# Kernel tuning notes

Measured on AMD Instinct MI355X. Metric: run time of the kernel, lower is better.

Reference implementation:

```python
import jax, jax.numpy as jnp
import numpy as np

# norse.LIFCell default parameters
DT = 1e-3
TAU_SYN_INV = 200.0   # 1 / 5e-3
TAU_MEM_INV = 100.0   # 1 / 1e-2
V_TH = 1.0
V_LEAK = 0.0
V_RESET = 0.0
ALPHA = 100.0         # SuperSpike surrogate slope

T, B, N_IN, N_HIDDEN, N_OUT = 16, 4096, 784, 256, 10


@jax.custom_vjp
def heaviside(x):
    return (x > 0).astype(x.dtype)

def _h_fwd(x):
    return heaviside(x), x

def _h_bwd(x, g):
    # SuperSpike surrogate: d/dx H(x) ~ 1 / (alpha*|x| + 1)^2
    return (g / (ALPHA * jnp.abs(x) + 1.0) ** 2,)

heaviside.defvjp(_h_fwd, _h_bwd)


def lif_step(inp, v, i):
    """One norse lif_step: Euler-integrate v and i, spike, hard reset."""
    v_decayed = v + DT * TAU_MEM_INV * ((V_LEAK - v) + i)
    i_decayed = i - DT * TAU_SYN_INV * i
    z = heaviside(v_decayed - V_TH)
    v_new = (1.0 - z) * v_decayed + z * V_RESET
    i_new = i_decayed + inp
    return z, v_new, i_new


def setup_inputs() -> dict:
    key = jax.random.key(0)
    k1, k2, k3, k4, k5 = jax.random.split(key, 5)
    # binary spike trains (T, B, N_IN)
    spike_input = (jax.random.uniform(k1, (T, B, N_IN)) < 0.3).astype(jnp.float32)
    lim1 = float(1.0 / np.sqrt(N_IN))
    lim2 = float(1.0 / np.sqrt(N_HIDDEN))
    W1 = jax.random.uniform(k2, (N_HIDDEN, N_IN), minval=-lim1, maxval=lim1, dtype=jnp.float32)
    b1 = jax.random.uniform(k3, (N_HIDDEN,), minval=-lim1, maxval=lim1, dtype=jnp.float32)
    W2 = jax.random.uniform(k4, (N_OUT, N_HIDDEN), minval=-lim2, maxval=lim2, dtype=jnp.float32)
    b2 = jax.random.uniform(k5, (N_OUT,), minval=-lim2, maxval=lim2, dtype=jnp.float32)
    return {"spike_input": spike_input, "W1": W1, "b1": b1, "W2": W2, "b2": b2}


def reference(spike_input, W1, b1, W2, b2):
    batch = spike_input.shape[1]
    nh, no = W1.shape[0], W2.shape[0]
    dtype = spike_input.dtype
    # LIFCell with state=None starts at v=v_leak, i=0
    init = (jnp.full((batch, nh), V_LEAK, dtype), jnp.zeros((batch, nh), dtype),
            jnp.full((batch, no), V_LEAK, dtype), jnp.zeros((batch, no), dtype))

    def step(carry, x_t):
        v1, i1, v2, i2 = carry
        c1 = x_t @ W1.T + b1                 # (B, N_HIDDEN)
        z1, v1, i1 = lif_step(c1, v1, i1)
        c2 = z1 @ W2.T + b2                  # (B, N_OUT)
        z2, v2, i2 = lif_step(c2, v2, i2)
        return (v1, i1, v2, i2), z2

    _, zs = jax.lax.scan(step, init, spike_input)  # zs: (T, B, N_OUT)
    return zs.sum(axis=0)                          # (B, N_OUT)
```

## Files before the change

### kernel.cpp

```cpp
#include <hip/hip_runtime.h>


#define T_STEPS 16
#define B_SZ    4096
#define N_IN    784
#define N_HID   256
#define N_OUT   10
#define M_TOT   (T_STEPS * B_SZ)
#define KPAD    800

typedef __bf16 bf16x8 __attribute__((ext_vector_type(8)));
typedef float  f32x4  __attribute__((ext_vector_type(4)));
typedef unsigned short ushort_t;

__device__ __forceinline__ unsigned short bf16_rne(float f) {
    unsigned u = __builtin_bit_cast(unsigned, f);
    u += 0x7fffu + ((u >> 16) & 1u);
    return (unsigned short)(u >> 16);
}

__global__ __launch_bounds__(256) void conv_w(
    const float* __restrict__ W1,
    unsigned short* __restrict__ Whi, unsigned short* __restrict__ Wlo)
{
    const int idx = blockIdx.x * 256 + threadIdx.x;
    if (idx >= N_HID * KPAD) return;
    const int n = idx / KPAD, k = idx % KPAD;
    unsigned short h = 0, l = 0;
    if (k < N_IN) {
        const float w = W1[n * N_IN + k];
        h = bf16_rne(w);
        const float hf = __builtin_bit_cast(float, (unsigned)h << 16);
        l = bf16_rne(w - hf);
    }
    Whi[idx] = h;
    Wlo[idx] = l;
}

__global__ __launch_bounds__(512, 4) void gemm1_mfma(
    const float* __restrict__ X,
    const unsigned short* __restrict__ Whi,
    const unsigned short* __restrict__ Wlo,
    const float* __restrict__ b1,
    float* __restrict__ C)
{
    __shared__ ushort_t As[2][128 * 32];
    __shared__ ushort_t Bh[2][256 * 32];
    __shared__ ushort_t Bl[2][256 * 32];

    const int tid  = threadIdx.x;
    const int lane = tid & 63;
    const int w    = tid >> 6;
    const int wm   = w >> 2;
    const int wn   = w & 3;
    const int m0   = blockIdx.x * 128;

    const int ar  = tid >> 2;
    const int ap  = tid & 3;
    const int acs = ap ^ (ar & 3);
    const float* aSrc = X + (size_t)(m0 + ar) * N_IN + acs * 8;

    f32x4 acc[4][4];
    #pragma unroll
    for (int i = 0; i < 4; ++i)
        #pragma unroll
        for (int j = 0; j < 4; ++j)
            #pragma unroll
            for (int q = 0; q < 4; ++q)
                acc[i][j][q] = 0.0f;

    auto stage = [&](int bi, int kt) {
        const int k0 = kt * 32;
        #pragma unroll
        for (int ii = 0; ii < 2; ++ii) {
            const int rb = w * 32 + ii * 16 + (lane >> 2);
            const int cs = (lane & 3) ^ (rb & 3);
            const size_t go = (size_t)rb * KPAD + k0 + cs * 8;
            ushort_t* dh = &Bh[bi][(w * 32 + ii * 16) * 32];
            ushort_t* dl = &Bl[bi][(w * 32 + ii * 16) * 32];
            __builtin_amdgcn_global_load_lds(
                (const __attribute__((address_space(1))) void*)(Whi + go),
                (__attribute__((address_space(3))) void*)dh, 16, 0, 0);
            __builtin_amdgcn_global_load_lds(
                (const __attribute__((address_space(1))) void*)(Wlo + go),
                (__attribute__((address_space(3))) void*)dl, 16, 0, 0);
        }
        const int kg = k0 + acs * 8;
        uint4 pk = make_uint4(0u, 0u, 0u, 0u);
        if (kg < N_IN) {
            const float4* s = reinterpret_cast<const float4*>(aSrc + k0);
            const float4 f0 = s[0];
            const float4 f1 = s[1];
            pk.x = (__builtin_bit_cast(unsigned, f0.x) >> 16) |
                   (__builtin_bit_cast(unsigned, f0.y) & 0xffff0000u);
            pk.y = (__builtin_bit_cast(unsigned, f0.z) >> 16) |
                   (__builtin_bit_cast(unsigned, f0.w) & 0xffff0000u);
            pk.z = (__builtin_bit_cast(unsigned, f1.x) >> 16) |
                   (__builtin_bit_cast(unsigned, f1.y) & 0xffff0000u);
            pk.w = (__builtin_bit_cast(unsigned, f1.z) >> 16) |
                   (__builtin_bit_cast(unsigned, f1.w) & 0xffff0000u);
        }
        *reinterpret_cast<uint4*>(&As[bi][ar * 32 + ap * 8]) = pk;
    };

    const int NT = KPAD / 32;
    int buf = 0;
    stage(0, 0);

    for (int kt = 0; kt < NT; ++kt) {
        __syncthreads();

        bf16x8 af[4];
        #pragma unroll
        for (int i = 0; i < 4; ++i) {
            const int r = wm * 64 + i * 16 + (lane & 15);
            const int p = (lane >> 4) ^ (r & 3);
            af[i] = *reinterpret_cast<const bf16x8*>(&As[buf][r * 32 + p * 8]);
        }
        bf16x8 bfr[4];
        #pragma unroll
        for (int j = 0; j < 4; ++j) {
            const int r = wn * 64 + j * 16 + (lane & 15);
            const int p = (lane >> 4) ^ (r & 3);
            bfr[j] = *reinterpret_cast<const bf16x8*>(&Bh[buf][r * 32 + p * 8]);
        }

        if (kt + 1 < NT) stage(buf ^ 1, kt + 1);

        #pragma unroll
        for (int i = 0; i < 4; ++i)
            #pragma unroll
            for (int j = 0; j < 4; ++j)
                acc[i][j] = __builtin_amdgcn_mfma_f32_16x16x32_bf16(
                    af[i], bfr[j], acc[i][j], 0, 0, 0);

        #pragma unroll
        for (int j = 0; j < 4; ++j) {
            const int r = wn * 64 + j * 16 + (lane & 15);
            const int p = (lane >> 4) ^ (r & 3);
            bfr[j] = *reinterpret_cast<const bf16x8*>(&Bl[buf][r * 32 + p * 8]);
        }
        #pragma unroll
        for (int i = 0; i < 4; ++i)
            #pragma unroll
            for (int j = 0; j < 4; ++j)
                acc[i][j] = __builtin_amdgcn_mfma_f32_16x16x32_bf16(
                    af[i], bfr[j], acc[i][j], 0, 0, 0);

        buf ^= 1;
    }

    #pragma unroll
    for (int j = 0; j < 4; ++j) {
        const int col  = wn * 64 + j * 16 + (lane & 15);
        const float bb = b1[col];
        #pragma unroll
        for (int i = 0; i < 4; ++i) {
            const int rbase = m0 + wm * 64 + i * 16 + ((lane >> 4) << 2);
            #pragma unroll
            for (int q = 0; q < 4; ++q)
                C[(size_t)(rbase + q) * N_HID + col] = acc[i][j][q] + bb;
        }
    }
}

__global__ __launch_bounds__(256) void lif1_kernel(float* __restrict__ C1)
{
    const int g = blockIdx.x * 256 + threadIdx.x;
    const size_t stride = (size_t)B_SZ * N_HID;
    float v = 0.0f, cur = 0.0f;
    #pragma unroll
    for (int t = 0; t < T_STEPS; ++t) {
        const size_t off = (size_t)t * stride + g;
        const float c = C1[off];
        const float vd = v + 0.1f * ((0.0f - v) + cur);
        const float id = cur - 0.2f * cur;
        const bool  sp = vd > 1.0f;
        C1[off] = sp ? 1.0f : 0.0f;
        v = sp ? 0.0f : vd;
        cur = id + c;
    }
}

__global__ __launch_bounds__(640) void gemm2_f32(
    const float* __restrict__ Z, const float* __restrict__ W2,
    const float* __restrict__ b2, float* __restrict__ C2)
{
    __shared__ float zs[64 * 268];
    __shared__ float ws[N_OUT * N_HID];
    const int tid = threadIdx.x;
    const int m0 = blockIdx.x * 64;

    for (int idx = tid; idx < 4096; idx += 640) {
        const int r = idx >> 6;
        const int c = (idx & 63) << 2;
        *(float4*)&zs[r * 268 + c] =
            *(const float4*)&Z[(size_t)(m0 + r) * N_HID + c];
    }
    *(float4*)&ws[tid * 4] = *(const float4*)&W2[tid * 4];
    __syncthreads();

    const int o = tid >> 6;
    const int r = tid & 63;
    float acc = b2[o];
    #pragma unroll
    for (int k = 0; k < N_HID; k += 4) {
        const float4 z4 = *(const float4*)&zs[r * 268 + k];
        const float4 w4 = *(const float4*)&ws[o * N_HID + k];
        acc += z4.x * w4.x + z4.y * w4.y + z4.z * w4.z + z4.w * w4.w;
    }
    C2[(size_t)(m0 + r) * N_OUT + o] = acc;
}

__global__ __launch_bounds__(256) void lif2_kernel(
    const float* __restrict__ C2, float* __restrict__ out)
{
    const int g = blockIdx.x * 256 + threadIdx.x;
    const int stride = B_SZ * N_OUT;
    float v = 0.0f, cur = 0.0f, s = 0.0f;
    #pragma unroll
    for (int t = 0; t < T_STEPS; ++t) {
        const float c = C2[t * stride + g];
        const float vd = v + 0.1f * ((0.0f - v) + cur);
        const float id = cur - 0.2f * cur;
        const bool  sp = vd > 1.0f;
        s += sp ? 1.0f : 0.0f;
        v = sp ? 0.0f : vd;
        cur = id + c;
    }
    out[g] = s;
}

extern "C" void kernel_launch(void* const* d_in, const int* in_sizes, int n_in,
                              void* d_out, int out_size, void* d_ws, size_t ws_size,
                              hipStream_t stream)
{
    const float* X  = (const float*)d_in[0];
    const float* W1 = (const float*)d_in[1];
    const float* b1 = (const float*)d_in[2];
    const float* W2 = (const float*)d_in[3];
    const float* b2 = (const float*)d_in[4];
    float* out = (float*)d_out;

    unsigned short* Whi = (unsigned short*)d_ws;
    unsigned short* Wlo = Whi + N_HID * KPAD;
    float* C1 = (float*)((char*)d_ws + (1 << 20));
    float* C2 = C1 + (size_t)M_TOT * N_HID;

    conv_w<<<(N_HID * KPAD + 255) / 256, 256, 0, stream>>>(W1, Whi, Wlo);

    gemm1_mfma<<<M_TOT / 128, 512, 0, stream>>>(X, Whi, Wlo, b1, C1);

    lif1_kernel<<<(B_SZ * N_HID) / 256, 256, 0, stream>>>(C1);

    gemm2_f32<<<M_TOT / 64, 640, 0, stream>>>(C1, W2, b2, C2);

    lif2_kernel<<<(B_SZ * N_OUT) / 256, 256, 0, stream>>>(C2, out);
}
```

Before: 132.1 us.

## Load GEMM1 operands directly from global into registers, dropping LDS staging

After: 216.6 us. 1.64x slower.

```diff
diff --git a/kernel.cpp b/kernel.cpp
--- a/kernel.cpp
+++ b/kernel.cpp
@@ -8,20 +8,22 @@
 #define N_OUT   10
 #define M_TOT   (T_STEPS * B_SZ)
 #define KPAD    800
+#define BKS     32
 
 typedef __bf16 bf16x8 __attribute__((ext_vector_type(8)));
 typedef float  f32x4  __attribute__((ext_vector_type(4)));
 typedef unsigned short ushort_t;
+typedef unsigned int   u32;
 
 __device__ __forceinline__ unsigned short bf16_rne(float f) {
-    unsigned u = __builtin_bit_cast(unsigned, f);
+    u32 u = __builtin_bit_cast(u32, f);
     u += 0x7fffu + ((u >> 16) & 1u);
     return (unsigned short)(u >> 16);
 }
 
 __global__ __launch_bounds__(256) void conv_w(
     const float* __restrict__ W1,
-    unsigned short* __restrict__ Whi, unsigned short* __restrict__ Wlo)
+    ushort_t* __restrict__ Whi, ushort_t* __restrict__ Wlo)
 {
     const int idx = blockIdx.x * 256 + threadIdx.x;
     if (idx >= N_HID * KPAD) return;
@@ -30,35 +32,46 @@
     if (k < N_IN) {
         const float w = W1[n * N_IN + k];
         h = bf16_rne(w);
-        const float hf = __builtin_bit_cast(float, (unsigned)h << 16);
+        const float hf = __builtin_bit_cast(float, (u32)h << 16);
         l = bf16_rne(w - hf);
     }
     Whi[idx] = h;
     Wlo[idx] = l;
 }
 
-__global__ __launch_bounds__(512, 4) void gemm1_mfma(
+__device__ __forceinline__ u32 pack_hi16(u32 a, u32 b) {
+    return (a >> 16) | (b & 0xffff0000u);
+}
+
+__global__ __launch_bounds__(512, 2) void gemm1_mfma(
     const float* __restrict__ X,
-    const unsigned short* __restrict__ Whi,
-    const unsigned short* __restrict__ Wlo,
+    const ushort_t* __restrict__ Whi,
+    const ushort_t* __restrict__ Wlo,
     const float* __restrict__ b1,
     float* __restrict__ C)
 {
-    __shared__ ushort_t As[2][128 * 32];
-    __shared__ ushort_t Bh[2][256 * 32];
-    __shared__ ushort_t Bl[2][256 * 32];
-
     const int tid  = threadIdx.x;
     const int lane = tid & 63;
     const int w    = tid >> 6;
     const int wm   = w >> 2;
     const int wn   = w & 3;
     const int m0   = blockIdx.x * 128;
-
-    const int ar  = tid >> 2;
-    const int ap  = tid & 3;
-    const int acs = ap ^ (ar & 3);
-    const float* aSrc = X + (size_t)(m0 + ar) * N_IN + acs * 8;
+    const int ls   = lane >> 4;
+    const int lr   = lane & 15;
+
+    const float* aP[4];
+    #pragma unroll
+    for (int i = 0; i < 4; ++i)
+        aP[i] = X + (size_t)(m0 + wm * 64 + i * 16 + lr) * N_IN + ls * 8;
+
+    const ushort_t* bhP[4];
+    const ushort_t* blP[4];
+    #pragma unroll
+    for (int j = 0; j < 4; ++j) {
+        const size_t ro = (size_t)(wn * 64 + j * 16 + lr) * KPAD + ls * 8;
+        bhP[j] = Whi + ro;
+        blP[j] = Wlo + ro;
+    }
 
     f32x4 acc[4][4];
     #pragma unroll
@@ -69,94 +82,55 @@
             for (int q = 0; q < 4; ++q)
                 acc[i][j][q] = 0.0f;
 
-    auto stage = [&](int bi, int kt) {
-        const int k0 = kt * 32;
-        #pragma unroll
-        for (int ii = 0; ii < 2; ++ii) {
-            const int rb = w * 32 + ii * 16 + (lane >> 2);
-            const int cs = (lane & 3) ^ (rb & 3);
-            const size_t go = (size_t)rb * KPAD + k0 + cs * 8;
-            ushort_t* dh = &Bh[bi][(w * 32 + ii * 16) * 32];
-            ushort_t* dl = &Bl[bi][(w * 32 + ii * 16) * 32];
-            __builtin_amdgcn_global_load_lds(
-                (const __attribute__((address_space(1))) void*)(Whi + go),
-                (__attribute__((address_space(3))) void*)dh, 16, 0, 0);
-            __builtin_amdgcn_global_load_lds(
-                (const __attribute__((address_space(1))) void*)(Wlo + go),
-                (__attribute__((address_space(3))) void*)dl, 16, 0, 0);
+    auto kstep = [&](int kt, bool tail) {
+        const int k0 = kt * BKS;
+        bf16x8 af[4];
+        #pragma unroll
+        for (int i = 0; i < 4; ++i) {
+            uint4 pk = make_uint4(0u, 0u, 0u, 0u);
+            if (!tail || ls < 2) {
+                const uint4* s = reinterpret_cast<const uint4*>(aP[i] + k0);
+                const uint4 q0 = s[0];
+                const uint4 q1 = s[1];
+                pk.x = pack_hi16(q0.x, q0.y);
+                pk.y = pack_hi16(q0.z, q0.w);
+                pk.z = pack_hi16(q1.x, q1.y);
+                pk.w = pack_hi16(q1.z, q1.w);
+            }
+            af[i] = __builtin_bit_cast(bf16x8, pk);
         }
-        const int kg = k0 + acs * 8;
-        uint4 pk = make_uint4(0u, 0u, 0u, 0u);
-        if (kg < N_IN) {
-            const float4* s = reinterpret_cast<const float4*>(aSrc + k0);
-            const float4 f0 = s[0];
-            const float4 f1 = s[1];
-            pk.x = (__builtin_bit_cast(unsigned, f0.x) >> 16) |
-                   (__builtin_bit_cast(unsigned, f0.y) & 0xffff0000u);
-            pk.y = (__builtin_bit_cast(unsigned, f0.z) >> 16) |
-                   (__builtin_bit_cast(unsigned, f0.w) & 0xffff0000u);
-            pk.z = (__builtin_bit_cast(unsigned, f1.x) >> 16) |
-                   (__builtin_bit_cast(unsigned, f1.y) & 0xffff0000u);
-            pk.w = (__builtin_bit_cast(unsigned, f1.z) >> 16) |
-                   (__builtin_bit_cast(unsigned, f1.w) & 0xffff0000u);
+        bf16x8 bh[4], bl[4];
+        #pragma unroll
+        for (int j = 0; j < 4; ++j) {
+            bh[j] = *reinterpret_cast<const bf16x8*>(bhP[j] + k0);
+            bl[j] = *reinterpret_cast<const bf16x8*>(blP[j] + k0);
         }
-        *reinterpret_cast<uint4*>(&As[bi][ar * 32 + ap * 8]) = pk;
-    };
-
-    const int NT = KPAD / 32;
-    int buf = 0;
-    stage(0, 0);
-
-    for (int kt = 0; kt < NT; ++kt) {
-        __syncthreads();
-
-        bf16x8 af[4];
-        #pragma unroll
-        for (int i = 0; i < 4; ++i) {
-            const int r = wm * 64 + i * 16 + (lane & 15);
-            const int p = (lane >> 4) ^ (r & 3);
-            af[i] = *reinterpret_cast<const bf16x8*>(&As[buf][r * 32 + p * 8]);
-        }
-        bf16x8 bfr[4];
-        #pragma unroll
-        for (int j = 0; j < 4; ++j) {
-            const int r = wn * 64 + j * 16 + (lane & 15);
-            const int p = (lane >> 4) ^ (r & 3);
-            bfr[j] = *reinterpret_cast<const bf16x8*>(&Bh[buf][r * 32 + p * 8]);
-        }
-
-        if (kt + 1 < NT) stage(buf ^ 1, kt + 1);
-
         #pragma unroll
         for (int i = 0; i < 4; ++i)
             #pragma unroll
             for (int j = 0; j < 4; ++j)
                 acc[i][j] = __builtin_amdgcn_mfma_f32_16x16x32_bf16(
-                    af[i], bfr[j], acc[i][j], 0, 0, 0);
-
-        #pragma unroll
-        for (int j = 0; j < 4; ++j) {
-            const int r = wn * 64 + j * 16 + (lane & 15);
-            const int p = (lane >> 4) ^ (r & 3);
-            bfr[j] = *reinterpret_cast<const bf16x8*>(&Bl[buf][r * 32 + p * 8]);
-        }
+                    af[i], bh[j], acc[i][j], 0, 0, 0);
         #pragma unroll
         for (int i = 0; i < 4; ++i)
             #pragma unroll
             for (int j = 0; j < 4; ++j)
                 acc[i][j] = __builtin_amdgcn_mfma_f32_16x16x32_bf16(
-                    af[i], bfr[j], acc[i][j], 0, 0, 0);
-
-        buf ^= 1;
-    }
+                    af[i], bl[j], acc[i][j], 0, 0, 0);
+    };
+
+    #pragma unroll 4
+    for (int kt = 0; kt < 24; ++kt)
+        kstep(kt, false);
+    kstep(24, true);
 
     #pragma unroll
     for (int j = 0; j < 4; ++j) {
-        const int col  = wn * 64 + j * 16 + (lane & 15);
+        const int col  = wn * 64 + j * 16 + lr;
         const float bb = b1[col];
         #pragma unroll
         for (int i = 0; i < 4; ++i) {
-            const int rbase = m0 + wm * 64 + i * 16 + ((lane >> 4) << 2);
+            const int rbase = m0 + wm * 64 + i * 16 + (ls << 2);
             #pragma unroll
             for (int q = 0; q < 4; ++q)
                 C[(size_t)(rbase + q) * N_HID + col] = acc[i][j][q] + bb;
@@ -242,8 +216,8 @@
     const float* b2 = (const float*)d_in[4];
     float* out = (float*)d_out;
 
-    unsigned short* Whi = (unsigned short*)d_ws;
-    unsigned short* Wlo = Whi + N_HID * KPAD;
+    ushort_t* Whi = (ushort_t*)d_ws;
+    ushort_t* Wlo = Whi + N_HID * KPAD;
     float* C1 = (float*)((char*)d_ws + (1 << 20));
     float* C2 = C1 + (size_t)M_TOT * N_HID;
 
```
